# Kernel tuning notes

Measured on AMD Instinct MI355X. Metric: run time of the kernel, lower is better.

The kernel has to match this reference:

```python
import jax, jax.numpy as jnp
import numpy as np

N_NODES = 100000
N_EDGES = 1600000
D_FEAT = 128


def sage_conv(x, src, dst, Wl, Wr, b, n_nodes):
    # gather source features, mean-aggregate at destination (PyG SAGEConv, aggr='mean')
    msgs = x[src]                                            # [E, d]
    agg_sum = jax.ops.segment_sum(msgs, dst, num_segments=n_nodes)
    cnt = jax.ops.segment_sum(jnp.ones((src.shape[0],), dtype=x.dtype), dst,
                              num_segments=n_nodes)
    mean = agg_sum / jnp.maximum(cnt, 1.0)[:, None]
    return mean @ Wl + x @ Wr + b


def setup_inputs() -> dict:
    key = jax.random.key(0)
    ks = jax.random.split(key, 9)
    def w(k, shape):
        fan_in = shape[0]
        return jax.random.normal(k, shape, dtype=jnp.float32) / np.sqrt(fan_in)
    x = jax.random.normal(ks[0], (N_NODES, D_FEAT), dtype=jnp.float32)
    edge_index = jax.random.randint(ks[1], (2, N_EDGES), 0, N_NODES, dtype=jnp.int64)
    return {
        "x": x,
        "edge_index": edge_index,
        "W1l": w(ks[2], (D_FEAT, 64)), "W1r": w(ks[3], (D_FEAT, 64)), "b1": jnp.zeros((64,), jnp.float32),
        "W2l": w(ks[4], (64, 128)),    "W2r": w(ks[5], (64, 128)),    "b2": jnp.zeros((128,), jnp.float32),
        "W3l": w(ks[6], (128, 64)),    "W3r": w(ks[7], (128, 64)),    "b3": jnp.zeros((64,), jnp.float32),
        "Wlin": w(ks[8], (64, 10)),    "blin": jnp.zeros((10,), jnp.float32),
    }


def reference(x, edge_index, W1l, W1r, b1, W2l, W2r, b2, W3l, W3r, b3, Wlin, blin):
    n = x.shape[0]
    src, dst = edge_index[0], edge_index[1]
    # dropout omitted (evaluated in inference / identity form)
    h = jnp.tanh(sage_conv(x, src, dst, W1l, W1r, b1, n))
    h = jnp.tanh(sage_conv(h, src, dst, W2l, W2r, b2, n))
    h = jnp.tanh(sage_conv(h, src, dst, W3l, W3r, b3, n))
    return h @ Wlin + blin
```

## Files before the change

### kernel.cpp

```cpp
#include <hip/hip_runtime.h>

#define THREADS 256
#define NB 256
#define NB_SHIFT 8
#define TILE_E 1024
#define EPT 2
#define BMAXPAD 512
#define WT_LD 136

typedef unsigned short ushort_t;
typedef __attribute__((ext_vector_type(8))) short bf16x8;
typedef __attribute__((ext_vector_type(4))) float f32x4;

__device__ __forceinline__ unsigned short f2bf(float f) {
    unsigned u = __float_as_uint(f);
    u += 0x7fff + ((u >> 16) & 1);
    return (unsigned short)(u >> 16);
}
__device__ __forceinline__ float bf2f(unsigned short s) {
    return __uint_as_float((unsigned)s << 16);
}
__device__ __forceinline__ float4 bf4_to_f4(ushort4 u) {
    return make_float4(bf2f(u.x), bf2f(u.y), bf2f(u.z), bf2f(u.w));
}
__device__ __forceinline__ ushort4 f4_to_bf4(float4 v) {
    ushort4 o;
    o.x = f2bf(v.x); o.y = f2bf(v.y); o.z = f2bf(v.z); o.w = f2bf(v.w);
    return o;
}
__device__ __forceinline__ unsigned pack_bf2(float a, float b) {
    return (unsigned)f2bf(a) | ((unsigned)f2bf(b) << 16);
}
__device__ __forceinline__ void acc_pair(unsigned u, float& lo, float& hi) {
    lo += __uint_as_float(u << 16);
    hi += __uint_as_float(u);
}

__global__ __launch_bounds__(64)
void detect_kernel(const unsigned* __restrict__ ei_words, int* __restrict__ flag) {
    if (threadIdx.x == 0 && blockIdx.x == 0) {
        int allzero = 1;
        for (int i = 0; i < 64; ++i) {
            if (ei_words[2 * i + 1] != 0u) { allzero = 0; break; }
        }
        *flag = allzero;
    }
}

__device__ __forceinline__ void load_edge(const void* ei, int is64, int E, int i,
                                          int& s, int& t) {
    if (is64) {
        const long long* p = (const long long*)ei;
        s = (int)p[i];
        t = (int)p[E + i];
    } else {
        const int* p = (const int*)ei;
        s = p[i];
        t = p[E + i];
    }
}

__global__ __launch_bounds__(512)
void tilesort_kernel(const void* __restrict__ ei, const int* __restrict__ flag,
                     unsigned* __restrict__ tbuf, int* __restrict__ tcnt,
                     int* __restrict__ tstart, int E, int B) {
    __shared__ int hist[BMAXPAD];
    __shared__ int wsum[8];
    const int t   = blockIdx.x;
    const int e0  = t * TILE_E;
    const int is64 = *flag;
    unsigned w[EPT];
    unsigned short bk[EPT];
    hist[threadIdx.x] = 0;
    __syncthreads();
#pragma unroll
    for (int k = 0; k < EPT; ++k) {
        const int i = e0 + k * 512 + (int)threadIdx.x;
        bk[k] = 0xFFFFu;
        w[k]  = 0u;
        if (i < E) {
            int s, d;
            load_edge(ei, is64, E, i, s, d);
            w[k]  = (unsigned)s | ((unsigned)(d & (NB - 1)) << 17);
            bk[k] = (unsigned short)(d >> NB_SHIFT);
            atomicAdd(&hist[bk[k]], 1);
        }
    }
    __syncthreads();
    const int lane = threadIdx.x & 63;
    const int wid  = threadIdx.x >> 6;
    const int v = hist[threadIdx.x];
    int incl = v;
#pragma unroll
    for (int off = 1; off < 64; off <<= 1) {
        int tt = __shfl_up(incl, off, 64);
        if (lane >= off) incl += tt;
    }
    if (lane == 63) wsum[wid] = incl;
    __syncthreads();
    int woff = 0;
    for (int ww = 0; ww < wid; ++ww) woff += wsum[ww];
    const int excl = woff + incl - v;
    hist[threadIdx.x] = excl;
    const int b = threadIdx.x;
    if (b < B) { tcnt[(size_t)t * B + b] = v; tstart[(size_t)t * B + b] = excl; }
    __syncthreads();
#pragma unroll
    for (int k = 0; k < EPT; ++k) {
        if (bk[k] != 0xFFFFu) {
            const int pos = atomicAdd(&hist[bk[k]], 1);
            tbuf[(size_t)t * TILE_E + pos] = w[k];
        }
    }
}

__global__ __launch_bounds__(256)
void transpose2_kernel(const int* __restrict__ tcnt, const int* __restrict__ tstart,
                       int* __restrict__ tcntT, int* __restrict__ tstartT,
                       int T, int B) {
    __shared__ int ta[32][33];
    __shared__ int tb[32][33];
    const int bx = blockIdx.x;
    const int by = blockIdx.y;
    const int tx = threadIdx.x & 31;
    const int ty = threadIdx.x >> 5;
#pragma unroll
    for (int r = 0; r < 4; ++r) {
        const int trow = by * 32 + ty * 4 + r;
        const int bcol = bx * 32 + tx;
        if (trow < T && bcol < B) {
            ta[ty * 4 + r][tx] = tcnt[(size_t)trow * B + bcol];
            tb[ty * 4 + r][tx] = tstart[(size_t)trow * B + bcol];
        }
    }
    __syncthreads();
#pragma unroll
    for (int r = 0; r < 4; ++r) {
        const int brow = bx * 32 + ty * 4 + r;
        const int tcol = by * 32 + tx;
        if (brow < B && tcol < T) {
            tcntT[(size_t)brow * T + tcol]   = ta[tx][ty * 4 + r];
            tstartT[(size_t)brow * T + tcol] = tb[tx][ty * 4 + r];
        }
    }
}

__global__ __launch_bounds__(256)
void scan_partial_kernel(const int* __restrict__ cnt, int* __restrict__ bsum, int n) {
    const int base = blockIdx.x * 1024;
    int v = 0;
    for (int i = threadIdx.x; i < 1024; i += 256) {
        const int idx = base + i;
        v += (idx < n) ? cnt[idx] : 0;
    }
#pragma unroll
    for (int off = 32; off > 0; off >>= 1) v += __shfl_down(v, off, 64);
    __shared__ int ws[4];
    if ((threadIdx.x & 63) == 0) ws[threadIdx.x >> 6] = v;
    __syncthreads();
    if (threadIdx.x == 0) bsum[blockIdx.x] = ws[0] + ws[1] + ws[2] + ws[3];
}

__global__ __launch_bounds__(1024)
void scan_bsum_kernel(int* __restrict__ bsum, int* __restrict__ total, int nb) {
    __shared__ int wsum[16];
    const int lane = threadIdx.x & 63;
    const int wid  = threadIdx.x >> 6;
    int run = 0;
    for (int base = 0; base < nb; base += 1024) {
        const int i = base + (int)threadIdx.x;
        const int v = (i < nb) ? bsum[i] : 0;
        int incl = v;
#pragma unroll
        for (int off = 1; off < 64; off <<= 1) {
            int t = __shfl_up(incl, off, 64);
            if (lane >= off) incl += t;
        }
        if (lane == 63) wsum[wid] = incl;
        __syncthreads();
        if (wid == 0) {
            int wv = (lane < 16) ? wsum[lane] : 0;
#pragma unroll
            for (int off = 1; off < 16; off <<= 1) {
                int t = __shfl_up(wv, off, 64);
                if (lane >= off) wv += t;
            }
            if (lane < 16) wsum[lane] = wv;
        }
        __syncthreads();
        const int wbase = (wid > 0) ? wsum[wid - 1] : 0;
        const int tot   = wsum[15];
        if (i < nb) bsum[i] = run + wbase + incl - v;
        run += tot;
        __syncthreads();
    }
    if (threadIdx.x == 0) *total = run;
}

__global__ __launch_bounds__(256)
void scan_final_kernel(const int* __restrict__ cnt, const int* __restrict__ bsum,
                       int* __restrict__ outp, int n) {
    const int base = blockIdx.x * 1024 + threadIdx.x * 4;
    int a0 = 0, a1 = 0, a2 = 0, a3 = 0;
    if (base + 0 < n) a0 = cnt[base + 0];
    if (base + 1 < n) a1 = cnt[base + 1];
    if (base + 2 < n) a2 = cnt[base + 2];
    if (base + 3 < n) a3 = cnt[base + 3];
    const int mysum = a0 + a1 + a2 + a3;
    const int lane = threadIdx.x & 63;
    const int wid  = threadIdx.x >> 6;
    int incl = mysum;
#pragma unroll
    for (int off = 1; off < 64; off <<= 1) {
        int t = __shfl_up(incl, off, 64);
        if (lane >= off) incl += t;
    }
    __shared__ int ws[4];
    if (lane == 63) ws[wid] = incl;
    __syncthreads();
    int woff = 0;
    for (int w = 0; w < wid; ++w) woff += ws[w];
    int pre = bsum[blockIdx.x] + woff + (incl - mysum);
    if (base + 0 < n) outp[base + 0] = pre; pre += a0;
    if (base + 1 < n) outp[base + 1] = pre; pre += a1;
    if (base + 2 < n) outp[base + 2] = pre; pre += a2;
    if (base + 3 < n) outp[base + 3] = pre;
}

__global__ __launch_bounds__(512)
void finesort_kernel(const unsigned* __restrict__ tbuf, const int* __restrict__ tcntT,
                     const int* __restrict__ tstartT, const int* __restrict__ hbase,
                     int* __restrict__ rowptr, int* __restrict__ esrc,
                     int n, int E, int T, int B) {
    __shared__ int hist[NB];
    __shared__ int wsum[4];
    const int b  = blockIdx.x;
    const int e0 = hbase[(size_t)b * T];
    if (threadIdx.x < NB) hist[threadIdx.x] = 0;
    __syncthreads();
    for (int t = threadIdx.x; t < T; t += 512) {
        const int c  = tcntT[(size_t)b * T + t];
        const int ls = tstartT[(size_t)b * T + t];
        const unsigned* __restrict__ src = tbuf + (size_t)t * TILE_E + ls;
        for (int k = 0; k < c; ++k) atomicAdd(&hist[src[k] >> 17], 1);
    }
    __syncthreads();
    if (threadIdx.x < NB) {
        const int lane = threadIdx.x & 63;
        const int wid  = threadIdx.x >> 6;
        const int v = hist[threadIdx.x];
        int incl = v;
#pragma unroll
        for (int off = 1; off < 64; off <<= 1) {
            int tt = __shfl_up(incl, off, 64);
            if (lane >= off) incl += tt;
        }
        if (lane == 63) wsum[wid] = incl;
    }
    __syncthreads();
    if (threadIdx.x < NB) {
        const int wid = threadIdx.x >> 6;
        const int v   = hist[threadIdx.x];
        const int lane = threadIdx.x & 63;
        int incl = v;
#pragma unroll
        for (int off = 1; off < 64; off <<= 1) {
            int tt = __shfl_up(incl, off, 64);
            if (lane >= off) incl += tt;
        }
        int woff = 0;
        for (int w = 0; w < wid; ++w) woff += wsum[w];
        const int excl = woff + incl - v;
        hist[threadIdx.x] = e0 + excl;
        const int node = b * NB + (int)threadIdx.x;
        if (node < n) rowptr[node] = e0 + excl;
    }
    if (b == 0 && threadIdx.x == 0) rowptr[n] = E;
    __syncthreads();
    for (int t = threadIdx.x; t < T; t += 512) {
        const int c  = tcntT[(size_t)b * T + t];
        const int ls = tstartT[(size_t)b * T + t];
        const unsigned* __restrict__ src = tbuf + (size_t)t * TILE_E + ls;
        for (int k = 0; k < c; ++k) {
            const unsigned wv = src[k];
            const int pos = atomicAdd(&hist[wv >> 17], 1);
            esrc[pos] = (int)((wv & 0x1FFFFu) << 8);
        }
    }
}

__global__ __launch_bounds__(256)
void pack_dual_kernel(const float* __restrict__ Wl, const float* __restrict__ Wr,
                      ushort_t* __restrict__ WT) {
    int i = blockIdx.x * 256 + threadIdx.x;
    if (i >= 128 * 128) return;
    int k = i >> 7, c = i & 127;
    float v = (c < 64) ? Wl[k * 64 + c] : Wr[k * 64 + (c - 64)];
    WT[c * WT_LD + k] = f2bf(v);
}
__global__ __launch_bounds__(256)
void pack_stack_kernel(const float* __restrict__ Wl, const float* __restrict__ Wr,
                       ushort_t* __restrict__ WT) {
    int i = blockIdx.x * 256 + threadIdx.x;
    if (i >= 128 * 128) return;
    int k = i >> 7, c = i & 127;
    float v = (k < 64) ? Wl[k * 128 + c] : Wr[(k - 64) * 128 + c];
    WT[c * WT_LD + k] = f2bf(v);
}

template <bool A_FP32, bool TANH_BIAS>
__global__ __launch_bounds__(256)
void mfma_gemm_kernel(const void* __restrict__ Av, const ushort_t* __restrict__ WT,
                      const float* __restrict__ bias, ushort_t* __restrict__ C, int n) {
    __shared__ ushort_t sW[128 * WT_LD];
    {
        const uint4* gsrc = (const uint4*)WT;
        uint4* ldst = (uint4*)sW;
        for (int i = threadIdx.x; i < 128 * WT_LD * 2 / 16; i += 256) ldst[i] = gsrc[i];
    }
    __syncthreads();
    const int lane = threadIdx.x & 63;
    const int wave = threadIdx.x >> 6;
    const int kg   = lane >> 4;
    const int row0 = blockIdx.x * 64 + wave * 16;
    const int rA   = min(row0 + (lane & 15), n - 1);

    bf16x8 a[4];
    if (A_FP32) {
        const float* A = (const float*)Av;
#pragma unroll
        for (int t = 0; t < 4; ++t) {
            const float4 lo = *(const float4*)(A + (size_t)rA * 128 + t * 32 + kg * 8);
            const float4 hi = *(const float4*)(A + (size_t)rA * 128 + t * 32 + kg * 8 + 4);
            const ushort4 u0 = f4_to_bf4(lo), u1 = f4_to_bf4(hi);
            bf16x8 av;
            av[0] = (short)u0.x; av[1] = (short)u0.y; av[2] = (short)u0.z; av[3] = (short)u0.w;
            av[4] = (short)u1.x; av[5] = (short)u1.y; av[6] = (short)u1.z; av[7] = (short)u1.w;
            a[t] = av;
        }
    } else {
        const ushort_t* A = (const ushort_t*)Av;
#pragma unroll
        for (int t = 0; t < 4; ++t)
            a[t] = *(const bf16x8*)(A + (size_t)rA * 128 + t * 32 + kg * 8);
    }

    f32x4 acc[8];
#pragma unroll
    for (int ct = 0; ct < 8; ++ct) acc[ct] = (f32x4)(0.f);

#pragma unroll
    for (int ct = 0; ct < 8; ++ct) {
        const int c0 = ct * 16 + (lane & 15);
#pragma unroll
        for (int t = 0; t < 4; ++t) {
            const bf16x8 b = *(const bf16x8*)(sW + (size_t)c0 * WT_LD + t * 32 + kg * 8);
            acc[ct] = __builtin_amdgcn_mfma_f32_16x16x32_bf16(b, a[t], acc[ct], 0, 0, 0);
        }
    }

    const int r = row0 + (lane & 15);
    if (r < n) {
        ushort_t* crow = C + (size_t)r * 128 + kg * 4;
#pragma unroll
        for (int ct = 0; ct < 8; ++ct) {
            float v0 = acc[ct][0], v1 = acc[ct][1], v2 = acc[ct][2], v3 = acc[ct][3];
            if (TANH_BIAS) {
                const float4 bv = *(const float4*)(bias + ct * 16 + kg * 4);
                v0 = tanhf(v0 + bv.x); v1 = tanhf(v1 + bv.y);
                v2 = tanhf(v2 + bv.z); v3 = tanhf(v3 + bv.w);
            }
            uint2 pk;
            pk.x = pack_bf2(v0, v1);
            pk.y = pack_bf2(v2, v3);
            *(uint2*)(crow + ct * 16) = pk;
        }
    }
}

template <int OUTMODE>
__global__ __launch_bounds__(THREADS)
void gather_fuse_kernel(const int* __restrict__ rowptr, const int* __restrict__ esrc,
                        const ushort_t* __restrict__ pq, const float* __restrict__ bias,
                        ushort_t* __restrict__ hout, int n) {
    constexpr int CH  = 16;
    constexpr int NPB = THREADS / CH;
    const int node = blockIdx.x * NPB + (int)(threadIdx.x / CH);
    const int c    = threadIdx.x & (CH - 1);
    if (node >= n) return;
    const int begin = rowptr[node];
    const int end   = rowptr[node + 1];
    const char* __restrict__ base = (const char*)pq + 8 * c;
    float ax = 0.f, ay = 0.f, az = 0.f, aw = 0.f;
    int e = begin;
    for (; e + 8 <= end; e += 8) {
        uint2 d[8];
#pragma unroll
        for (int j = 0; j < 8; ++j) d[j] = *(const uint2*)(base + esrc[e + j]);
#pragma unroll
        for (int j = 0; j < 8; ++j) { acc_pair(d[j].x, ax, ay); acc_pair(d[j].y, az, aw); }
    }
    if (e + 4 <= end) {
        uint2 d[4];
#pragma unroll
        for (int j = 0; j < 4; ++j) d[j] = *(const uint2*)(base + esrc[e + j]);
#pragma unroll
        for (int j = 0; j < 4; ++j) { acc_pair(d[j].x, ax, ay); acc_pair(d[j].y, az, aw); }
        e += 4;
    }
    for (; e < end; ++e) {
        const uint2 d = *(const uint2*)(base + esrc[e]);
        acc_pair(d.x, ax, ay); acc_pair(d.y, az, aw);
    }
    const float inv = 1.0f / fmaxf((float)(end - begin), 1.0f);
    const float4 qv = bf4_to_f4(*(const ushort4*)(pq + (size_t)node * 128 + 64 + 4 * c));
    const float4 bv = *(const float4*)(bias + 4 * c);
    float4 o;
    o.x = tanhf(ax * inv + qv.x + bv.x);
    o.y = tanhf(ay * inv + qv.y + bv.y);
    o.z = tanhf(az * inv + qv.z + bv.z);
    o.w = tanhf(aw * inv + qv.w + bv.w);
    if (OUTMODE == 0) {
        *(ushort4*)(hout + (size_t)node * 128 + 64 + 4 * c) = f4_to_bf4(o);
    } else {
        *(ushort4*)(hout + (size_t)node * 64 + 4 * c) = f4_to_bf4(o);
    }
}

__global__ __launch_bounds__(THREADS)
void gather_mean_kernel(const int* __restrict__ rowptr, const int* __restrict__ esrc,
                        ushort_t* __restrict__ ah, int n) {
    constexpr int CH  = 16;
    constexpr int NPB = THREADS / CH;
    const int node = blockIdx.x * NPB + (int)(threadIdx.x / CH);
    const int c    = threadIdx.x & (CH - 1);
    if (node >= n) return;
    const int begin = rowptr[node];
    const int end   = rowptr[node + 1];
    const char* __restrict__ base = (const char*)ah + 128 + 8 * c;
    float ax = 0.f, ay = 0.f, az = 0.f, aw = 0.f;
    int e = begin;
    for (; e + 8 <= end; e += 8) {
        uint2 d[8];
#pragma unroll
        for (int j = 0; j < 8; ++j) d[j] = *(const uint2*)(base + esrc[e + j]);
#pragma unroll
        for (int j = 0; j < 8; ++j) { acc_pair(d[j].x, ax, ay); acc_pair(d[j].y, az, aw); }
    }
    if (e + 4 <= end) {
        uint2 d[4];
#pragma unroll
        for (int j = 0; j < 4; ++j) d[j] = *(const uint2*)(base + esrc[e + j]);
#pragma unroll
        for (int j = 0; j < 4; ++j) { acc_pair(d[j].x, ax, ay); acc_pair(d[j].y, az, aw); }
        e += 4;
    }
    for (; e < end; ++e) {
        const uint2 d = *(const uint2*)(base + esrc[e]);
        acc_pair(d.x, ax, ay); acc_pair(d.y, az, aw);
    }
    const float inv = 1.0f / fmaxf((float)(end - begin), 1.0f);
    ushort4 o = f4_to_bf4(make_float4(ax * inv, ay * inv, az * inv, aw * inv));
    *(ushort4*)(ah + (size_t)node * 128 + 4 * c) = o;
}

__global__ __launch_bounds__(THREADS)
void head_kernel(const ushort_t* __restrict__ h, const float* __restrict__ W,
                 const float* __restrict__ bias, float* __restrict__ out, int n) {
    __shared__ float sW[64 * 10];
    __shared__ float sb[10];
    for (int i = threadIdx.x; i < 640; i += THREADS) sW[i] = W[i];
    if (threadIdx.x < 10) sb[threadIdx.x] = bias[threadIdx.x];
    __syncthreads();
    int idx = blockIdx.x * THREADS + threadIdx.x;
    if (idx >= n * 10) return;
    int row = idx / 10;
    int col = idx - row * 10;
    const uint4* __restrict__ hr = (const uint4*)(h + (size_t)row * 64);
    float acc = sb[col];
#pragma unroll
    for (int k4 = 0; k4 < 8; ++k4) {
        const uint4 u = hr[k4];
        const float* w = sW + (8 * k4) * 10 + col;
        acc += __uint_as_float(u.x << 16)          * w[0];
        acc += __uint_as_float(u.x & 0xffff0000u)  * w[10];
        acc += __uint_as_float(u.y << 16)          * w[20];
        acc += __uint_as_float(u.y & 0xffff0000u)  * w[30];
        acc += __uint_as_float(u.z << 16)          * w[40];
        acc += __uint_as_float(u.z & 0xffff0000u)  * w[50];
        acc += __uint_as_float(u.w << 16)          * w[60];
        acc += __uint_as_float(u.w & 0xffff0000u)  * w[70];
    }
    out[idx] = acc;
}

extern "C" void kernel_launch(void* const* d_in, const int* in_sizes, int n_in,
                              void* d_out, int out_size, void* d_ws, size_t ws_size,
                              hipStream_t stream) {
    const float* x    = (const float*)d_in[0];
    const void*  ei   = d_in[1];
    const float* W1l  = (const float*)d_in[2];
    const float* W1r  = (const float*)d_in[3];
    const float* b1   = (const float*)d_in[4];
    const float* W2l  = (const float*)d_in[5];
    const float* W2r  = (const float*)d_in[6];
    const float* b2   = (const float*)d_in[7];
    const float* W3l  = (const float*)d_in[8];
    const float* W3r  = (const float*)d_in[9];
    const float* b3   = (const float*)d_in[10];
    const float* Wlin = (const float*)d_in[11];
    const float* blin = (const float*)d_in[12];
    float* out = (float*)d_out;

    const int n = in_sizes[0] / 128;
    const int E = in_sizes[1] / 2;
    const int B = (n + NB - 1) / NB;
    const int T = (E + TILE_E - 1) / TILE_E;
    const int Ctot = B * T;

    char* ws = (char*)d_ws;
    size_t off = 0;
    auto carve = [&](size_t bytes) {
        void* p = ws + off;
        off += (bytes + 255) & ~(size_t)255;
        return p;
    };
    int*      flag    = (int*)     carve(256);
    int*      bsum    = (int*)     carve(8192);
    unsigned* tbuf    = (unsigned*)carve((size_t)T * TILE_E * 4);
    int*      tcnt    = (int*)     carve((size_t)Ctot * 4);
    int*      tstart  = (int*)     carve((size_t)Ctot * 4);
    int*      tcntT   = (int*)     carve((size_t)Ctot * 4);
    int*      tstartT = (int*)     carve((size_t)Ctot * 4);
    int*      hbase   = (int*)     carve((size_t)(Ctot + 1) * 4);
    int*      rowptr  = (int*)     carve((size_t)(n + 1) * 4);
    int*      esrc    = (int*)     carve((size_t)E * 4);
    ushort_t* WT1     = (ushort_t*)carve((size_t)128 * WT_LD * 2);
    ushort_t* WT2     = (ushort_t*)carve((size_t)128 * WT_LD * 2);
    ushort_t* WT3     = (ushort_t*)carve((size_t)128 * WT_LD * 2);
    ushort_t* pq      = (ushort_t*)carve((size_t)n * 128 * 2);
    ushort_t* ah      = (ushort_t*)carve((size_t)n * 128 * 2);
    ushort_t* h2      = (ushort_t*)carve((size_t)n * 128 * 2);
    ushort_t* h3      = (ushort_t*)carve((size_t)n * 64 * 2);
    (void)ws_size;

    const int cscan   = (Ctot + 1023) / 1024;
    const int gblocks = (n + 63) / 64;

    pack_dual_kernel <<<64, 256, 0, stream>>>(W1l, W1r, WT1);
    pack_stack_kernel<<<64, 256, 0, stream>>>(W2l, W2r, WT2);
    pack_dual_kernel <<<64, 256, 0, stream>>>(W3l, W3r, WT3);

    detect_kernel<<<1, 64, 0, stream>>>((const unsigned*)ei, flag);
    tilesort_kernel<<<T, 512, 0, stream>>>(ei, flag, tbuf, tcnt, tstart, E, B);
    {
        dim3 tg((B + 31) / 32, (T + 31) / 32);
        transpose2_kernel<<<tg, 256, 0, stream>>>(tcnt, tstart, tcntT, tstartT, T, B);
    }
    scan_partial_kernel<<<cscan, 256, 0, stream>>>(tcntT, bsum, Ctot);
    scan_bsum_kernel<<<1, 1024, 0, stream>>>(bsum, hbase + Ctot, cscan);
    scan_final_kernel<<<cscan, 256, 0, stream>>>(tcntT, bsum, hbase, Ctot);
    finesort_kernel<<<B, 512, 0, stream>>>(tbuf, tcntT, tstartT, hbase,
                                           rowptr, esrc, n, E, T, B);

    mfma_gemm_kernel<true, false><<<gblocks, 256, 0, stream>>>(x, WT1, nullptr, pq, n);
    gather_fuse_kernel<0><<<(n + 15) / 16, THREADS, 0, stream>>>(
        rowptr, esrc, pq, b1, ah, n);

    gather_mean_kernel<<<(n + 15) / 16, THREADS, 0, stream>>>(rowptr, esrc, ah, n);
    mfma_gemm_kernel<false, true><<<gblocks, 256, 0, stream>>>(ah, WT2, b2, h2, n);

    mfma_gemm_kernel<false, false><<<gblocks, 256, 0, stream>>>(h2, WT3, nullptr, pq, n);
    gather_fuse_kernel<1><<<(n + 15) / 16, THREADS, 0, stream>>>(
        rowptr, esrc, pq, b3, h3, n);

    head_kernel<<<(n * 10 + THREADS - 1) / THREADS, THREADS, 0, stream>>>(
        h3, Wlin, blin, out, n);
}
```

Measured before the change: 245.8 us.

## Split interleaved feature buffers into compact 64-wide arrays and fuse head into gather

The interleaved 128-wide p|q and agg|h buffers become separate 64-wide bf16 arrays. Edge source offsets are now scaled by 128 bytes instead of 256, so each gathered row touches a denser buffer, which should improve cache locality for the random gathers. The final linear head is folded into the last gather kernel through a 16-lane shuffle reduction, which removes one kernel launch and the h3 round trip. The cost is extra shuffle work and 10 per-lane Wlin reads from global memory in the last gather.

```diff
diff --git a/kernel.cpp b/kernel.cpp
--- a/kernel.cpp
+++ b/kernel.cpp
@@ -284,7 +284,7 @@
         for (int k = 0; k < c; ++k) {
             const unsigned wv = src[k];
             const int pos = atomicAdd(&hist[wv >> 17], 1);
-            esrc[pos] = (int)((wv & 0x1FFFFu) << 8);
+            esrc[pos] = (int)((wv & 0x1FFFFu) << 7);
         }
     }
 }
@@ -308,10 +308,11 @@
     WT[c * WT_LD + k] = f2bf(v);
 }
 
-template <bool A_FP32, bool TANH_BIAS>
+template <int AMODE, bool TANH_BIAS, bool OUT_SPLIT>
 __global__ __launch_bounds__(256)
-void mfma_gemm_kernel(const void* __restrict__ Av, const ushort_t* __restrict__ WT,
-                      const float* __restrict__ bias, ushort_t* __restrict__ C, int n) {
+void mfma_gemm_kernel(const void* __restrict__ Av1, const void* __restrict__ Av2,
+                      const ushort_t* __restrict__ WT, const float* __restrict__ bias,
+                      ushort_t* __restrict__ C1, ushort_t* __restrict__ C2, int n) {
     __shared__ ushort_t sW[128 * WT_LD];
     {
         const uint4* gsrc = (const uint4*)WT;
@@ -326,8 +327,8 @@
     const int rA   = min(row0 + (lane & 15), n - 1);
 
     bf16x8 a[4];
-    if (A_FP32) {
-        const float* A = (const float*)Av;
+    if (AMODE == 0) {
+        const float* A = (const float*)Av1;
 #pragma unroll
         for (int t = 0; t < 4; ++t) {
             const float4 lo = *(const float4*)(A + (size_t)rA * 128 + t * 32 + kg * 8);
@@ -338,8 +339,15 @@
             av[4] = (short)u1.x; av[5] = (short)u1.y; av[6] = (short)u1.z; av[7] = (short)u1.w;
             a[t] = av;
         }
+    } else if (AMODE == 1) {
+        const ushort_t* A1 = (const ushort_t*)Av1;
+        const ushort_t* A2 = (const ushort_t*)Av2;
+        a[0] = *(const bf16x8*)(A1 + (size_t)rA * 64 + 0 + kg * 8);
+        a[1] = *(const bf16x8*)(A1 + (size_t)rA * 64 + 32 + kg * 8);
+        a[2] = *(const bf16x8*)(A2 + (size_t)rA * 64 + 0 + kg * 8);
+        a[3] = *(const bf16x8*)(A2 + (size_t)rA * 64 + 32 + kg * 8);
     } else {
-        const ushort_t* A = (const ushort_t*)Av;
+        const ushort_t* A = (const ushort_t*)Av1;
 #pragma unroll
         for (int t = 0; t < 4; ++t)
             a[t] = *(const bf16x8*)(A + (size_t)rA * 128 + t * 32 + kg * 8);
@@ -361,7 +369,6 @@
 
     const int r = row0 + (lane & 15);
     if (r < n) {
-        ushort_t* crow = C + (size_t)r * 128 + kg * 4;
 #pragma unroll
         for (int ct = 0; ct < 8; ++ct) {
             float v0 = acc[ct][0], v1 = acc[ct][1], v2 = acc[ct][2], v3 = acc[ct][3];
@@ -373,16 +380,25 @@
             uint2 pk;
             pk.x = pack_bf2(v0, v1);
             pk.y = pack_bf2(v2, v3);
-            *(uint2*)(crow + ct * 16) = pk;
-        }
-    }
-}
-
-template <int OUTMODE>
+            if (OUT_SPLIT) {
+                if (ct < 4)
+                    *(uint2*)(C1 + (size_t)r * 64 + kg * 4 + ct * 16) = pk;
+                else
+                    *(uint2*)(C2 + (size_t)r * 64 + kg * 4 + (ct - 4) * 16) = pk;
+            } else {
+                *(uint2*)(C1 + (size_t)r * 128 + kg * 4 + ct * 16) = pk;
+            }
+        }
+    }
+}
+
+template <int MODE>
 __global__ __launch_bounds__(THREADS)
 void gather_fuse_kernel(const int* __restrict__ rowptr, const int* __restrict__ esrc,
-                        const ushort_t* __restrict__ pq, const float* __restrict__ bias,
-                        ushort_t* __restrict__ hout, int n) {
+                        const ushort_t* __restrict__ p, const ushort_t* __restrict__ q,
+                        const float* __restrict__ bias, ushort_t* __restrict__ h1out,
+                        const float* __restrict__ Wlin, const float* __restrict__ blin,
+                        float* __restrict__ out, int n) {
     constexpr int CH  = 16;
     constexpr int NPB = THREADS / CH;
     const int node = blockIdx.x * NPB + (int)(threadIdx.x / CH);
@@ -390,7 +406,7 @@
     if (node >= n) return;
     const int begin = rowptr[node];
     const int end   = rowptr[node + 1];
-    const char* __restrict__ base = (const char*)pq + 8 * c;
+    const char* __restrict__ base = (const char*)p + 8 * c;
     float ax = 0.f, ay = 0.f, az = 0.f, aw = 0.f;
     int e = begin;
     for (; e + 8 <= end; e += 8) {
@@ -413,23 +429,41 @@
         acc_pair(d.x, ax, ay); acc_pair(d.y, az, aw);
     }
     const float inv = 1.0f / fmaxf((float)(end - begin), 1.0f);
-    const float4 qv = bf4_to_f4(*(const ushort4*)(pq + (size_t)node * 128 + 64 + 4 * c));
+    const float4 qv = bf4_to_f4(*(const ushort4*)(q + (size_t)node * 64 + 4 * c));
     const float4 bv = *(const float4*)(bias + 4 * c);
     float4 o;
     o.x = tanhf(ax * inv + qv.x + bv.x);
     o.y = tanhf(ay * inv + qv.y + bv.y);
     o.z = tanhf(az * inv + qv.z + bv.z);
     o.w = tanhf(aw * inv + qv.w + bv.w);
-    if (OUTMODE == 0) {
-        *(ushort4*)(hout + (size_t)node * 128 + 64 + 4 * c) = f4_to_bf4(o);
+    if (MODE == 0) {
+        *(ushort4*)(h1out + (size_t)node * 64 + 4 * c) = f4_to_bf4(o);
     } else {
-        *(ushort4*)(hout + (size_t)node * 64 + 4 * c) = f4_to_bf4(o);
+        float tot[10];
+        const float* __restrict__ w0 = Wlin + (4 * c + 0) * 10;
+        const float* __restrict__ w1 = Wlin + (4 * c + 1) * 10;
+        const float* __restrict__ w2 = Wlin + (4 * c + 2) * 10;
+        const float* __restrict__ w3 = Wlin + (4 * c + 3) * 10;
+#pragma unroll
+        for (int j = 0; j < 10; ++j)
+            tot[j] = o.x * w0[j] + o.y * w1[j] + o.z * w2[j] + o.w * w3[j];
+#pragma unroll
+        for (int m = 1; m < 16; m <<= 1) {
+#pragma unroll
+            for (int j = 0; j < 10; ++j) tot[j] += __shfl_xor(tot[j], m, 64);
+        }
+        if (c == 0) {
+            float* orow = out + (size_t)node * 10;
+#pragma unroll
+            for (int j = 0; j < 10; ++j) orow[j] = tot[j] + blin[j];
+        }
     }
 }
 
 __global__ __launch_bounds__(THREADS)
 void gather_mean_kernel(const int* __restrict__ rowptr, const int* __restrict__ esrc,
-                        ushort_t* __restrict__ ah, int n) {
+                        const ushort_t* __restrict__ h1, ushort_t* __restrict__ agg,
+                        int n) {
     constexpr int CH  = 16;
     constexpr int NPB = THREADS / CH;
     const int node = blockIdx.x * NPB + (int)(threadIdx.x / CH);
@@ -437,7 +471,7 @@
     if (node >= n) return;
     const int begin = rowptr[node];
     const int end   = rowptr[node + 1];
-    const char* __restrict__ base = (const char*)ah + 128 + 8 * c;
+    const char* __restrict__ base = (const char*)h1 + 8 * c;
     float ax = 0.f, ay = 0.f, az = 0.f, aw = 0.f;
     int e = begin;
     for (; e + 8 <= end; e += 8) {
@@ -461,37 +495,7 @@
     }
     const float inv = 1.0f / fmaxf((float)(end - begin), 1.0f);
     ushort4 o = f4_to_bf4(make_float4(ax * inv, ay * inv, az * inv, aw * inv));
-    *(ushort4*)(ah + (size_t)node * 128 + 4 * c) = o;
-}
-
-__global__ __launch_bounds__(THREADS)
-void head_kernel(const ushort_t* __restrict__ h, const float* __restrict__ W,
-                 const float* __restrict__ bias, float* __restrict__ out, int n) {
-    __shared__ float sW[64 * 10];
-    __shared__ float sb[10];
-    for (int i = threadIdx.x; i < 640; i += THREADS) sW[i] = W[i];
-    if (threadIdx.x < 10) sb[threadIdx.x] = bias[threadIdx.x];
-    __syncthreads();
-    int idx = blockIdx.x * THREADS + threadIdx.x;
-    if (idx >= n * 10) return;
-    int row = idx / 10;
-    int col = idx - row * 10;
-    const uint4* __restrict__ hr = (const uint4*)(h + (size_t)row * 64);
-    float acc = sb[col];
-#pragma unroll
-    for (int k4 = 0; k4 < 8; ++k4) {
-        const uint4 u = hr[k4];
-        const float* w = sW + (8 * k4) * 10 + col;
-        acc += __uint_as_float(u.x << 16)          * w[0];
-        acc += __uint_as_float(u.x & 0xffff0000u)  * w[10];
-        acc += __uint_as_float(u.y << 16)          * w[20];
-        acc += __uint_as_float(u.y & 0xffff0000u)  * w[30];
-        acc += __uint_as_float(u.z << 16)          * w[40];
-        acc += __uint_as_float(u.z & 0xffff0000u)  * w[50];
-        acc += __uint_as_float(u.w << 16)          * w[60];
-        acc += __uint_as_float(u.w & 0xffff0000u)  * w[70];
-    }
-    out[idx] = acc;
+    *(ushort4*)(agg + (size_t)node * 64 + 4 * c) = o;
 }
 
 extern "C" void kernel_launch(void* const* d_in, const int* in_sizes, int n_in,
@@ -538,10 +542,11 @@
     ushort_t* WT1     = (ushort_t*)carve((size_t)128 * WT_LD * 2);
     ushort_t* WT2     = (ushort_t*)carve((size_t)128 * WT_LD * 2);
     ushort_t* WT3     = (ushort_t*)carve((size_t)128 * WT_LD * 2);
-    ushort_t* pq      = (ushort_t*)carve((size_t)n * 128 * 2);
-    ushort_t* ah      = (ushort_t*)carve((size_t)n * 128 * 2);
+    ushort_t* p       = (ushort_t*)carve((size_t)n * 64 * 2);
+    ushort_t* q       = (ushort_t*)carve((size_t)n * 64 * 2);
+    ushort_t* h1      = (ushort_t*)carve((size_t)n * 64 * 2);
+    ushort_t* agg     = (ushort_t*)carve((size_t)n * 64 * 2);
     ushort_t* h2      = (ushort_t*)carve((size_t)n * 128 * 2);
-    ushort_t* h3      = (ushort_t*)carve((size_t)n * 64 * 2);
     (void)ws_size;
 
     const int cscan   = (Ctot + 1023) / 1024;
@@ -563,17 +568,17 @@
     finesort_kernel<<<B, 512, 0, stream>>>(tbuf, tcntT, tstartT, hbase,
                                            rowptr, esrc, n, E, T, B);
 
-    mfma_gemm_kernel<true, false><<<gblocks, 256, 0, stream>>>(x, WT1, nullptr, pq, n);
+    mfma_gemm_kernel<0, false, true><<<gblocks, 256, 0, stream>>>(
+        x, nullptr, WT1, nullptr, p, q, n);
     gather_fuse_kernel<0><<<(n + 15) / 16, THREADS, 0, stream>>>(
-        rowptr, esrc, pq, b1, ah, n);
-
-    gather_mean_kernel<<<(n + 15) / 16, THREADS, 0, stream>>>(rowptr, esrc, ah, n);
-    mfma_gemm_kernel<false, true><<<gblocks, 256, 0, stream>>>(ah, WT2, b2, h2, n);
-
-    mfma_gemm_kernel<false, false><<<gblocks, 256, 0, stream>>>(h2, WT3, nullptr, pq, n);
+        rowptr, esrc, p, q, b1, h1, nullptr, nullptr, nullptr, n);
+
+    gather_mean_kernel<<<(n + 15) / 16, THREADS, 0, stream>>>(rowptr, esrc, h1, agg, n);
+    mfma_gemm_kernel<1, true, false><<<gblocks, 256, 0, stream>>>(
+        agg, h1, WT2, b2, h2, nullptr, n);
+
+    mfma_gemm_kernel<2, false, true><<<gblocks, 256, 0, stream>>>(
+        h2, nullptr, WT3, nullptr, p, q, n);
     gather_fuse_kernel<1><<<(n + 15) / 16, THREADS, 0, stream>>>(
-        rowptr, esrc, pq, b3, h3, n);
-
-    head_kernel<<<(n * 10 + THREADS - 1) / THREADS, THREADS, 0, stream>>>(
-        h3, Wlin, blin, out, n);
-}
+        rowptr, esrc, p, q, b3, nullptr, Wlin, blin, out, n);
+}
```

Measured after the change: 244.9 us. No clear change (-0.4%).

## Fuse final linear head into last gather kernel and shrink gather unroll

Applied to the files above, without the earlier changes.

The final 64x10 linear layer is folded into the layer-3 gather kernel. Each 16-lane node group computes partial dot products from its 4 features against Wlin held in shared memory, reduces them with xor shuffles, and writes the 10 outputs directly. This removes the h3 intermediate buffer round trip and one kernel launch. Separately, the gather loops drop from 8-wide plus 4-wide unrolling to a plain 4-wide unroll, which lowers register pressure but may reduce memory-level parallelism. The fused epilogue adds a shared-memory load, a block barrier and shuffle reductions to every block.

```diff
diff --git a/kernel.cpp b/kernel.cpp
--- a/kernel.cpp
+++ b/kernel.cpp
@@ -378,13 +378,22 @@
     }
 }
 
-template <int OUTMODE>
+template <int MODE>
 __global__ __launch_bounds__(THREADS)
 void gather_fuse_kernel(const int* __restrict__ rowptr, const int* __restrict__ esrc,
                         const ushort_t* __restrict__ pq, const float* __restrict__ bias,
-                        ushort_t* __restrict__ hout, int n) {
+                        ushort_t* __restrict__ hout,
+                        const float* __restrict__ Wlin, const float* __restrict__ blin,
+                        float* __restrict__ out, int n) {
     constexpr int CH  = 16;
     constexpr int NPB = THREADS / CH;
+    __shared__ float sW[MODE == 1 ? 640 : 1];
+    __shared__ float sb[MODE == 1 ? 10 : 1];
+    if (MODE == 1) {
+        for (int i = threadIdx.x; i < 640; i += THREADS) sW[i] = Wlin[i];
+        if (threadIdx.x < 10) sb[threadIdx.x] = blin[threadIdx.x];
+        __syncthreads();
+    }
     const int node = blockIdx.x * NPB + (int)(threadIdx.x / CH);
     const int c    = threadIdx.x & (CH - 1);
     if (node >= n) return;
@@ -393,20 +402,16 @@
     const char* __restrict__ base = (const char*)pq + 8 * c;
     float ax = 0.f, ay = 0.f, az = 0.f, aw = 0.f;
     int e = begin;
-    for (; e + 8 <= end; e += 8) {
-        uint2 d[8];
-#pragma unroll
-        for (int j = 0; j < 8; ++j) d[j] = *(const uint2*)(base + esrc[e + j]);
-#pragma unroll
-        for (int j = 0; j < 8; ++j) { acc_pair(d[j].x, ax, ay); acc_pair(d[j].y, az, aw); }
-    }
-    if (e + 4 <= end) {
-        uint2 d[4];
-#pragma unroll
-        for (int j = 0; j < 4; ++j) d[j] = *(const uint2*)(base + esrc[e + j]);
-#pragma unroll
-        for (int j = 0; j < 4; ++j) { acc_pair(d[j].x, ax, ay); acc_pair(d[j].y, az, aw); }
-        e += 4;
+    for (; e + 4 <= end; e += 4) {
+        const int o0 = esrc[e + 0], o1 = esrc[e + 1], o2 = esrc[e + 2], o3 = esrc[e + 3];
+        const uint2 d0 = *(const uint2*)(base + o0);
+        const uint2 d1 = *(const uint2*)(base + o1);
+        const uint2 d2 = *(const uint2*)(base + o2);
+        const uint2 d3 = *(const uint2*)(base + o3);
+        acc_pair(d0.x, ax, ay); acc_pair(d0.y, az, aw);
+        acc_pair(d1.x, ax, ay); acc_pair(d1.y, az, aw);
+        acc_pair(d2.x, ax, ay); acc_pair(d2.y, az, aw);
+        acc_pair(d3.x, ax, ay); acc_pair(d3.y, az, aw);
     }
     for (; e < end; ++e) {
         const uint2 d = *(const uint2*)(base + esrc[e]);
@@ -420,10 +425,27 @@
     o.y = tanhf(ay * inv + qv.y + bv.y);
     o.z = tanhf(az * inv + qv.z + bv.z);
     o.w = tanhf(aw * inv + qv.w + bv.w);
-    if (OUTMODE == 0) {
+    if (MODE == 0) {
         *(ushort4*)(hout + (size_t)node * 128 + 64 + 4 * c) = f4_to_bf4(o);
     } else {
-        *(ushort4*)(hout + (size_t)node * 64 + 4 * c) = f4_to_bf4(o);
+        float tot[10];
+        const float* __restrict__ w0 = sW + (4 * c + 0) * 10;
+        const float* __restrict__ w1 = sW + (4 * c + 1) * 10;
+        const float* __restrict__ w2 = sW + (4 * c + 2) * 10;
+        const float* __restrict__ w3 = sW + (4 * c + 3) * 10;
+#pragma unroll
+        for (int j = 0; j < 10; ++j)
+            tot[j] = o.x * w0[j] + o.y * w1[j] + o.z * w2[j] + o.w * w3[j];
+#pragma unroll
+        for (int m = 1; m < 16; m <<= 1) {
+#pragma unroll
+            for (int j = 0; j < 10; ++j) tot[j] += __shfl_xor(tot[j], m, 64);
+        }
+        if (c == 0) {
+            float* orow = out + (size_t)node * 10;
+#pragma unroll
+            for (int j = 0; j < 10; ++j) orow[j] = tot[j] + sb[j];
+        }
     }
 }
 
@@ -440,20 +462,16 @@
     const char* __restrict__ base = (const char*)ah + 128 + 8 * c;
     float ax = 0.f, ay = 0.f, az = 0.f, aw = 0.f;
     int e = begin;
-    for (; e + 8 <= end; e += 8) {
-        uint2 d[8];
-#pragma unroll
-        for (int j = 0; j < 8; ++j) d[j] = *(const uint2*)(base + esrc[e + j]);
-#pragma unroll
-        for (int j = 0; j < 8; ++j) { acc_pair(d[j].x, ax, ay); acc_pair(d[j].y, az, aw); }
-    }
-    if (e + 4 <= end) {
-        uint2 d[4];
-#pragma unroll
-        for (int j = 0; j < 4; ++j) d[j] = *(const uint2*)(base + esrc[e + j]);
-#pragma unroll
-        for (int j = 0; j < 4; ++j) { acc_pair(d[j].x, ax, ay); acc_pair(d[j].y, az, aw); }
-        e += 4;
+    for (; e + 4 <= end; e += 4) {
+        const int o0 = esrc[e + 0], o1 = esrc[e + 1], o2 = esrc[e + 2], o3 = esrc[e + 3];
+        const uint2 d0 = *(const uint2*)(base + o0);
+        const uint2 d1 = *(const uint2*)(base + o1);
+        const uint2 d2 = *(const uint2*)(base + o2);
+        const uint2 d3 = *(const uint2*)(base + o3);
+        acc_pair(d0.x, ax, ay); acc_pair(d0.y, az, aw);
+        acc_pair(d1.x, ax, ay); acc_pair(d1.y, az, aw);
+        acc_pair(d2.x, ax, ay); acc_pair(d2.y, az, aw);
+        acc_pair(d3.x, ax, ay); acc_pair(d3.y, az, aw);
     }
     for (; e < end; ++e) {
         const uint2 d = *(const uint2*)(base + esrc[e]);
@@ -462,36 +480,6 @@
     const float inv = 1.0f / fmaxf((float)(end - begin), 1.0f);
     ushort4 o = f4_to_bf4(make_float4(ax * inv, ay * inv, az * inv, aw * inv));
     *(ushort4*)(ah + (size_t)node * 128 + 4 * c) = o;
-}
-
-__global__ __launch_bounds__(THREADS)
-void head_kernel(const ushort_t* __restrict__ h, const float* __restrict__ W,
-                 const float* __restrict__ bias, float* __restrict__ out, int n) {
-    __shared__ float sW[64 * 10];
-    __shared__ float sb[10];
-    for (int i = threadIdx.x; i < 640; i += THREADS) sW[i] = W[i];
-    if (threadIdx.x < 10) sb[threadIdx.x] = bias[threadIdx.x];
-    __syncthreads();
-    int idx = blockIdx.x * THREADS + threadIdx.x;
-    if (idx >= n * 10) return;
-    int row = idx / 10;
-    int col = idx - row * 10;
-    const uint4* __restrict__ hr = (const uint4*)(h + (size_t)row * 64);
-    float acc = sb[col];
-#pragma unroll
-    for (int k4 = 0; k4 < 8; ++k4) {
-        const uint4 u = hr[k4];
-        const float* w = sW + (8 * k4) * 10 + col;
-        acc += __uint_as_float(u.x << 16)          * w[0];
-        acc += __uint_as_float(u.x & 0xffff0000u)  * w[10];
-        acc += __uint_as_float(u.y << 16)          * w[20];
-        acc += __uint_as_float(u.y & 0xffff0000u)  * w[30];
-        acc += __uint_as_float(u.z << 16)          * w[40];
-        acc += __uint_as_float(u.z & 0xffff0000u)  * w[50];
-        acc += __uint_as_float(u.w << 16)          * w[60];
-        acc += __uint_as_float(u.w & 0xffff0000u)  * w[70];
-    }
-    out[idx] = acc;
 }
 
 extern "C" void kernel_launch(void* const* d_in, const int* in_sizes, int n_in,
@@ -541,7 +529,6 @@
     ushort_t* pq      = (ushort_t*)carve((size_t)n * 128 * 2);
     ushort_t* ah      = (ushort_t*)carve((size_t)n * 128 * 2);
     ushort_t* h2      = (ushort_t*)carve((size_t)n * 128 * 2);
-    ushort_t* h3      = (ushort_t*)carve((size_t)n * 64 * 2);
     (void)ws_size;
 
     const int cscan   = (Ctot + 1023) / 1024;
@@ -565,15 +552,12 @@
 
     mfma_gemm_kernel<true, false><<<gblocks, 256, 0, stream>>>(x, WT1, nullptr, pq, n);
     gather_fuse_kernel<0><<<(n + 15) / 16, THREADS, 0, stream>>>(
-        rowptr, esrc, pq, b1, ah, n);
+        rowptr, esrc, pq, b1, ah, nullptr, nullptr, nullptr, n);
 
     gather_mean_kernel<<<(n + 15) / 16, THREADS, 0, stream>>>(rowptr, esrc, ah, n);
     mfma_gemm_kernel<false, true><<<gblocks, 256, 0, stream>>>(ah, WT2, b2, h2, n);
 
     mfma_gemm_kernel<false, false><<<gblocks, 256, 0, stream>>>(h2, WT3, nullptr, pq, n);
     gather_fuse_kernel<1><<<(n + 15) / 16, THREADS, 0, stream>>>(
-        rowptr, esrc, pq, b3, h3, n);
-
-    head_kernel<<<(n * 10 + THREADS - 1) / THREADS, THREADS, 0, stream>>>(
-        h3, Wlin, blin, out, n);
-}
+        rowptr, esrc, pq, b3, nullptr, Wlin, blin, out, n);
+}
```

Measured after the change: 249.8 us. No clear change (+1.6%).
